# Optimization experiments

Measured on AMD Instinct MI355X. Metric: run time of the kernel, lower is better.

## Reference

```python
import jax, jax.numpy as jnp
import numpy as np

NUM_HEADS = 4
D_MODEL = 256
HEAD_DIM = D_MODEL // NUM_HEADS  # 64
B, N = 4, 2048


def _pointwise_conv(w, b, x):
    # Conv1d(kernel_size=1): x [b, in, n] -> [b, out, n]
    return jnp.einsum('oi,bin->bon', w, x) + b[None, :, None]


def setup_inputs() -> dict:
    key = jax.random.key(0)
    ks = jax.random.split(key, 11)
    def g(k, shape, scale=1.0):
        return jax.random.normal(k, shape, dtype=jnp.float32) * scale
    return {
        'query': g(ks[0], (B, D_MODEL, N)),
        'key':   g(ks[1], (B, D_MODEL, N)),
        'value': g(ks[2], (B, D_MODEL, N)),
        'wq': g(ks[3], (D_MODEL, D_MODEL), 1.0 / np.sqrt(D_MODEL)),
        'bq': g(ks[4], (D_MODEL,), 0.02),
        'wk': g(ks[5], (D_MODEL, D_MODEL), 1.0 / np.sqrt(D_MODEL)),
        'bk': g(ks[6], (D_MODEL,), 0.02),
        'wv': g(ks[7], (D_MODEL, D_MODEL), 1.0 / np.sqrt(D_MODEL)),
        'bv': g(ks[8], (D_MODEL,), 0.02),
        'wm': g(ks[9], (D_MODEL, D_MODEL), 1.0 / np.sqrt(D_MODEL)),
        'bm': g(ks[10], (D_MODEL,), 0.02),
    }


def reference(query, key, value, wq, bq, wk, bk, wv, bv, wm, bm):
    b = query.shape[0]
    # Project and split heads: [b, d_model, n] -> [b, head_dim, heads, n]
    q = _pointwise_conv(wq, bq, query).reshape(b, HEAD_DIM, NUM_HEADS, -1)
    k = _pointwise_conv(wk, bk, key).reshape(b, HEAD_DIM, NUM_HEADS, -1)
    v = _pointwise_conv(wv, bv, value).reshape(b, HEAD_DIM, NUM_HEADS, -1)
    # scaled dot-product attention; scale is head dim (query.shape[1] in torch)
    scores = jnp.einsum('bdhn,bdhm->bhnm', q, k) / jnp.sqrt(jnp.float32(HEAD_DIM))
    prob = jax.nn.softmax(scores, axis=-1)
    x = jnp.einsum('bhnm,bdhm->bdhn', prob, v)
    # merge heads and final pointwise conv
    x = x.reshape(b, HEAD_DIM * NUM_HEADS, -1)
    return _pointwise_conv(wm, bm, x)
```

## Files before the change

kernel.cpp:

```cpp
#include <hip/hip_runtime.h>

typedef __attribute__((ext_vector_type(8))) short short8;
typedef __attribute__((ext_vector_type(4))) float f32x4;
typedef __attribute__((ext_vector_type(16))) float f32x16;

#define MFMA_B16(a, b, c) __builtin_amdgcn_mfma_f32_16x16x32_bf16((a), (b), (c), 0, 0, 0)
#define MFMA32(a, b, c) __builtin_amdgcn_mfma_f32_32x32x16_bf16((a), (b), (c), 0, 0, 0)

#define NTOK 2048
#define DM 256
#define NB4 4
#define HD 64

__device__ __forceinline__ short f2bf(float f) {
  union { float f; unsigned u; } x;
  x.f = f;
  unsigned r = x.u + 0x7fffu + ((x.u >> 16) & 1u);
  return (short)(r >> 16);
}
__device__ __forceinline__ float bf2f(short s) {
  union { unsigned u; float f; } x;
  x.u = ((unsigned)(unsigned short)s) << 16;
  return x.f;
}

__device__ __forceinline__ void gload16(const short* g, short* l) {
  __builtin_amdgcn_global_load_lds(
      (const __attribute__((address_space(1))) void*)g,
      (__attribute__((address_space(3))) void*)l, 16, 0, 0);
}

__global__ __launch_bounds__(256) void k_wpre(const float* __restrict__ w0,
    const float* __restrict__ w1, const float* __restrict__ w2,
    const float* __restrict__ w3, short* __restrict__ wbf) {
  int t = blockIdx.x * 256 + threadIdx.x;
  const float* ws4[4] = {w0, w1, w2, w3};
  int base = t * 32;
#pragma unroll
  for (int blk = 0; blk < 4; blk++) {
    int off = base + blk * 8;
    int tau = off >> 16;
    int rest = off & 65535;
    int c = rest >> 8, ip = rest & 255;
    const float* srow = ws4[tau] + (size_t)c * 256;
    short8 r;
#pragma unroll
    for (int j = 0; j < 8; j++) {
      int i2 = ip + j;
      r[j] = (tau == 3) ? f2bf(srow[4 * (i2 & 63) + (i2 >> 6)]) : f2bf(srow[i2]);
    }
    *(short8*)(wbf + off) = r;
  }
}

__global__ __launch_bounds__(256, 4) void k_proj(const float* __restrict__ q,
    const float* __restrict__ k, const float* __restrict__ v,
    const short* __restrict__ wbf, const float* __restrict__ bq,
    const float* __restrict__ bk, const float* __restrict__ bv,
    short* __restrict__ qt, short* __restrict__ kt, short* __restrict__ vt) {
  __shared__ __align__(16) short As[16384];
  int z = blockIdx.y, b = z & 3, tau = z >> 2;
  const float* src = ((tau == 0) ? q : (tau == 1) ? k : v) + (size_t)b * DM * NTOK;
  const short* W = wbf + (size_t)tau * 65536;
  const float* bias = (tau == 0) ? bq : (tau == 1) ? bk : bv;
  int n0 = blockIdx.x * 64;
  int t = threadIdx.x;
  {
    int nseg = t & 15, rg = t >> 4;
#pragma unroll
    for (int outer = 0; outer < 2; outer++) {
      int iG = rg + 16 * outer;
      const float* s0 = src + (size_t)(iG * 8) * NTOK + n0 + nseg * 4;
      float4 rows[8];
#pragma unroll
      for (int j = 0; j < 8; j++) rows[j] = *(const float4*)(s0 + (size_t)j * NTOK);
      int i32 = iG >> 2, fhi = iG & 3, s = iG & 7;
#pragma unroll
      for (int e = 0; e < 4; e++) {
        int n = nseg * 4 + e;
        int nb = n >> 4, flo = n & 15;
        short8 r;
#pragma unroll
        for (int j = 0; j < 8; j++)
          r[j] = f2bf(e == 0 ? rows[j].x : e == 1 ? rows[j].y
                                         : e == 2 ? rows[j].z : rows[j].w);
        int frag = ((nb * 8 + i32) * 64 + fhi * 16 + flo) ^ s;
        *(short8*)(As + frag * 8) = r;
      }
    }
  }
  __syncthreads();
  int lane = t & 63, w = t >> 6;
  int lo = lane & 15, hi = lane >> 4;
  f32x4 acc[4][4] = {};
  const short* wrow = W + (size_t)(64 * w + lo) * DM + hi * 8;
#pragma unroll
  for (int ks = 0; ks < 8; ks++) {
    int sr = hi | ((ks & 1) << 2);
    short8 xf[4];
#pragma unroll
    for (int nb = 0; nb < 4; nb++) {
      int frag = ((nb * 8 + ks) * 64 + lane) ^ sr;
      xf[nb] = *(const short8*)(As + frag * 8);
    }
#pragma unroll
    for (int cb = 0; cb < 4; cb++) {
      short8 wf = *(const short8*)(wrow + (size_t)cb * 16 * DM + ks * 32);
      if (tau < 2) {
#pragma unroll
        for (int nb = 0; nb < 4; nb++)
          acc[cb][nb] = MFMA_B16(xf[nb], wf, acc[cb][nb]);
      } else {
#pragma unroll
        for (int nb = 0; nb < 4; nb++)
          acc[cb][nb] = MFMA_B16(wf, xf[nb], acc[cb][nb]);
      }
    }
  }
  if (tau < 2) {
    short* out = tau ? kt : qt;
    float scale = tau ? 1.0f : (0.125f * 1.44269504f);
#pragma unroll
    for (int cb = 0; cb < 4; cb++) {
      int c = 64 * w + 16 * cb + lo;
      float bvv = bias[c];
      int h = c & 3, d = c >> 2;
      size_t base = (size_t)(b * 4 + h) * 64;
#pragma unroll
      for (int nb = 0; nb < 4; nb++) {
#pragma unroll
        for (int r = 0; r < 4; r++) {
          int n = n0 + 16 * nb + 4 * hi + r;
          size_t addr = (((base + (n >> 5)) * 4 + (d >> 4)) * 64 +
                         (n & 31) + 32 * ((d >> 3) & 1)) * 8 + (d & 7);
          out[addr] = f2bf((acc[cb][nb][r] + bvv) * scale);
        }
      }
    }
  } else {
#pragma unroll
    for (int cb = 0; cb < 4; cb++) {
#pragma unroll
      for (int r = 0; r < 4; r++) {
        int c = 64 * w + 16 * cb + 4 * hi + r;
        float bvv = bias[c];
        int h = c & 3, d = c >> 2;
        size_t base = (size_t)(b * 4 + h) * 128;
#pragma unroll
        for (int nb = 0; nb < 4; nb++) {
          int m = n0 + 16 * nb + lo;
          size_t addr = (((base + (m >> 4)) * 2 + (d >> 5)) * 64 +
                         (d & 31) + 32 * ((m >> 3) & 1)) * 8 + (m & 7);
          vt[addr] = f2bf(acc[cb][nb][r] + bvv);
        }
      }
    }
  }
}

template <int SPLIT>
__global__ __launch_bounds__(512, 4) void k_attn(const short* __restrict__ qt,
    const short* __restrict__ kt, const short* __restrict__ vt,
    short* __restrict__ opart, float* __restrict__ ml) {
  __shared__ __align__(16) short Ks[3][4096];
  __shared__ __align__(16) short Vs[3][4096];
  int b, h, chunk, n0;
  if (SPLIT == 4) {
    int bid = blockIdx.x;
    int xcd = bid & 7, slot = bid >> 3;
    int g = xcd + 8 * (slot >> 3);
    n0 = (slot & 7) * 256;
    h = g & 3;
    int zz = g >> 2;
    b = zz & 3;
    chunk = zz >> 2;
  } else {
    b = blockIdx.z & 3; chunk = 0; h = blockIdx.y; n0 = blockIdx.x * 256;
  }
  int tid = threadIdx.x;
  int lane = tid & 63, w = tid >> 6;
  int l31 = lane & 31, hi2 = lane >> 5;
  const int CH = NTOK / SPLIT;
  const int kv0 = chunk * CH;
  int bh = b * 4 + h;
  const short* Qf = qt + (size_t)bh * 131072;
  const short* Kf = kt + (size_t)bh * 131072;
  const short* Vf = vt + (size_t)bh * 131072;
  short8 qf[4];
#pragma unroll
  for (int dk = 0; dk < 4; dk++)
    qf[dk] = *(const short8*)(Qf + (((size_t)((n0 >> 5) + w) * 4 + dk) * 64 + lane) * 8);
  f32x16 acc[2] = {};
  float lacc = 0.0f;

  const int nt = CH >> 6;
  {
    int m0 = kv0;
    gload16(Kf + (size_t)(m0 >> 5) * 2048 + tid * 8, &Ks[0][tid * 8]);
    gload16(Vf + (size_t)(m0 >> 4) * 1024 + tid * 8, &Vs[0][tid * 8]);
    int m1 = kv0 + 64;
    gload16(Kf + (size_t)(m1 >> 5) * 2048 + tid * 8, &Ks[1][tid * 8]);
    gload16(Vf + (size_t)(m1 >> 4) * 1024 + tid * 8, &Vs[1][tid * 8]);
  }
  asm volatile("s_waitcnt vmcnt(0)" ::: "memory");
  __builtin_amdgcn_s_barrier();
  __builtin_amdgcn_sched_barrier(0);

#pragma unroll
  for (int t = 0; t < nt; t++) {
    int cur = t % 3;
    if (t + 2 < nt) {
      int m2 = kv0 + ((t + 2) << 6);
      int nxt = (t + 2) % 3;
      gload16(Kf + (size_t)(m2 >> 5) * 2048 + tid * 8, &Ks[nxt][tid * 8]);
      gload16(Vf + (size_t)(m2 >> 4) * 1024 + tid * 8, &Vs[nxt][tid * 8]);
    }
#pragma unroll
    for (int mb2 = 0; mb2 < 2; mb2++) {
      f32x16 s = {};
      __builtin_amdgcn_s_setprio(1);
#pragma unroll
      for (int dk = 0; dk < 4; dk++) {
        short8 kf = *(const short8*)&Ks[cur][(mb2 * 4 + dk) * 512 + lane * 8];
        s = MFMA32(kf, qf[dk], s);
      }
      __builtin_amdgcn_s_setprio(0);
#pragma unroll
      for (int ks = 0; ks < 2; ks++) {
        float e0 = exp2f(s[ks * 8 + 0]), e1 = exp2f(s[ks * 8 + 1]);
        float e2 = exp2f(s[ks * 8 + 2]), e3 = exp2f(s[ks * 8 + 3]);
        float e4 = exp2f(s[ks * 8 + 4]), e5 = exp2f(s[ks * 8 + 5]);
        float e6 = exp2f(s[ks * 8 + 6]), e7 = exp2f(s[ks * 8 + 7]);
        lacc += ((e0 + e1) + (e2 + e3)) + ((e4 + e5) + (e6 + e7));
        unsigned A, B, C2, D2;
        asm("v_cvt_pk_bf16_f32 %0, %1, %2" : "=v"(A) : "v"(e0), "v"(e1));
        asm("v_cvt_pk_bf16_f32 %0, %1, %2" : "=v"(C2) : "v"(e2), "v"(e3));
        asm("v_cvt_pk_bf16_f32 %0, %1, %2" : "=v"(B) : "v"(e4), "v"(e5));
        asm("v_cvt_pk_bf16_f32 %0, %1, %2" : "=v"(D2) : "v"(e6), "v"(e7));
        asm("v_permlane32_swap_b32 %0, %1" : "+v"(A), "+v"(B));
        asm("v_permlane32_swap_b32 %0, %1" : "+v"(C2), "+v"(D2));
        union { unsigned u[4]; short8 v8; } pu;
        pu.u[0] = A; pu.u[1] = C2; pu.u[2] = B; pu.u[3] = D2;
        __builtin_amdgcn_s_setprio(1);
#pragma unroll
        for (int dcol = 0; dcol < 2; dcol++) {
          short8 vf = *(const short8*)&Vs[cur][((mb2 * 2 + ks) * 2 + dcol) * 512 + lane * 8];
          acc[dcol] = MFMA32(pu.v8, vf, acc[dcol]);
        }
        __builtin_amdgcn_s_setprio(0);
      }
    }
    if (t + 1 < nt) {
      if (t + 2 < nt)
        asm volatile("s_waitcnt vmcnt(2) lgkmcnt(0)" ::: "memory");
      else
        asm volatile("s_waitcnt vmcnt(0) lgkmcnt(0)" ::: "memory");
      __builtin_amdgcn_s_barrier();
      __builtin_amdgcn_sched_barrier(0);
    }
  }

  float l = lacc + __shfl_xor(lacc, 32);
  size_t rbase = (((size_t)chunk * NB4 + b) * 4 + h) * NTOK;
  if (lane < 32) ml[rbase + n0 + 32 * w + lane] = l;
#pragma unroll
  for (int r = 0; r < 16; r++) {
    int n = n0 + 32 * w + (r & 3) + 8 * (r >> 2) + 4 * hi2;
#pragma unroll
    for (int dcol = 0; dcol < 2; dcol++)
      opart[(rbase + n) * HD + dcol * 32 + l31] = f2bf(acc[dcol][r]);
  }
}

template <int NCH>
__global__ __launch_bounds__(256, 4) void k_out(const short* __restrict__ W,
    const short* __restrict__ opart, const float* __restrict__ ml,
    const float* __restrict__ bias, float* __restrict__ outp) {
  __shared__ __align__(16) short As[8192];
  int b = blockIdx.y;
  int n0 = blockIdx.x * 32;
  int t = threadIdx.x;
  int lane = t & 63, w = t >> 6;
  int lo16 = lane & 15, hi = lane >> 4;
  {
    int d8 = t & 7, h = (t >> 3) & 3, nb8 = t >> 5;
    int i32 = 2 * h + (d8 >> 2), fhi = d8 & 3;
#pragma unroll
    for (int it = 0; it < 4; it++) {
      int noff = nb8 * 4 + it;
      int n = n0 + noff;
      int nb = noff >> 4, flo = noff & 15;
      size_t row0 = ((size_t)b * 4 + h) * NTOK + n;
      float l = ml[row0];
      float o[8];
      short8 o0 = *(const short8*)(opart + row0 * HD + d8 * 8);
#pragma unroll
      for (int j = 0; j < 8; j++) o[j] = bf2f(o0[j]);
#pragma unroll
      for (int ch = 1; ch < NCH; ch++) {
        size_t rowc = row0 + (size_t)ch * 16 * NTOK;
        l += ml[rowc];
        short8 oc = *(const short8*)(opart + rowc * HD + d8 * 8);
#pragma unroll
        for (int j = 0; j < 8; j++) o[j] += bf2f(oc[j]);
      }
      float inv = 1.0f / l;
      short8 res;
#pragma unroll
      for (int j = 0; j < 8; j++) res[j] = f2bf(o[j] * inv);
      int frag = ((nb * 8 + i32) * 64 + fhi * 16 + flo) ^ d8;
      *(short8*)(As + frag * 8) = res;
    }
  }
  __syncthreads();
  f32x4 acc[4][2] = {};
  const short* arow = W + (size_t)(64 * w + lo16) * DM + hi * 8;
#pragma unroll
  for (int ks = 0; ks < 8; ks++) {
    int sr = hi | ((ks & 1) << 2);
    short8 bbr[2];
#pragma unroll
    for (int nb = 0; nb < 2; nb++) {
      int frag = ((nb * 8 + ks) * 64 + lane) ^ sr;
      bbr[nb] = *(const short8*)(As + frag * 8);
    }
#pragma unroll
    for (int cb = 0; cb < 4; cb++) {
      short8 a = *(const short8*)(arow + (size_t)cb * 16 * DM + ks * 32);
#pragma unroll
      for (int nb = 0; nb < 2; nb++)
        acc[cb][nb] = MFMA_B16(a, bbr[nb], acc[cb][nb]);
    }
  }
#pragma unroll
  for (int cb = 0; cb < 4; cb++) {
#pragma unroll
    for (int r = 0; r < 4; r++) {
      int c = 64 * w + 16 * cb + 4 * hi + r;
      float bvv = bias[c];
#pragma unroll
      for (int nb = 0; nb < 2; nb++) {
        int n = n0 + 16 * nb + lo16;
        outp[((size_t)b * DM + c) * NTOK + n] = acc[cb][nb][r] + bvv;
      }
    }
  }
}

extern "C" void kernel_launch(void* const* d_in, const int* in_sizes, int n_in,
                              void* d_out, int out_size, void* d_ws, size_t ws_size,
                              hipStream_t stream) {
  const float* q  = (const float*)d_in[0];
  const float* k  = (const float*)d_in[1];
  const float* v  = (const float*)d_in[2];
  const float* wq = (const float*)d_in[3];
  const float* bq = (const float*)d_in[4];
  const float* wk = (const float*)d_in[5];
  const float* bk = (const float*)d_in[6];
  const float* wv = (const float*)d_in[7];
  const float* bv = (const float*)d_in[8];
  const float* wm = (const float*)d_in[9];
  const float* bm = (const float*)d_in[10];

  char* ws = (char*)d_ws;
  const size_t MB = 1024 * 1024;
  short* Qt  = (short*)(ws);
  short* Kt  = (short*)(ws + 4 * MB);
  short* Vt  = (short*)(ws + 8 * MB);
  short* Wbf = (short*)(ws + 12 * MB);
  float* ML    = (float*)(ws + 13 * MB);
  short* Opart = (short*)(ws + 14 * MB);

  k_wpre<<<dim3(32), 256, 0, stream>>>(wq, wk, wv, wm, Wbf);
  k_proj<<<dim3(32, 12), 256, 0, stream>>>(q, k, v, Wbf, bq, bk, bv, Qt, Kt, Vt);

  if (ws_size >= 32 * MB) {
    k_attn<4><<<dim3(512), 512, 0, stream>>>(Qt, Kt, Vt, Opart, ML);
    k_out<4><<<dim3(64, 4), 256, 0, stream>>>(Wbf + 3 * 65536, Opart, ML, bm, (float*)d_out);
  } else {
    k_attn<1><<<dim3(8, 4, 4), 512, 0, stream>>>(Qt, Kt, Vt, Opart, ML);
    k_out<1><<<dim3(64, 4), 256, 0, stream>>>(Wbf + 3 * 65536, Opart, ML, bm, (float*)d_out);
  }

  (void)in_sizes; (void)n_in; (void)out_size; (void)ws_size;
}
```

Measured before the change: 68.22 us.

## Fuse split-KV combine and output projection into attention via last-block counter

Removes the separate k_out launch on the split path. Each attention block atomically increments a per-(batch, query-tile) counter, and the last of the 16 contributing blocks (4 heads x 4 KV chunks) merges the partial outputs, normalizes them, and applies the output pointwise conv with bias directly to the output. This saves a kernel launch and the gap between the two kernels. In exchange it adds a memset, threadfences and atomics, and a serial tail in which only 32 of 512 blocks do the projection work.

```diff
diff --git a/kernel.cpp b/kernel.cpp
--- a/kernel.cpp
+++ b/kernel.cpp
@@ -161,9 +161,13 @@
 template <int SPLIT>
 __global__ __launch_bounds__(512, 4) void k_attn(const short* __restrict__ qt,
     const short* __restrict__ kt, const short* __restrict__ vt,
-    short* __restrict__ opart, float* __restrict__ ml) {
-  __shared__ __align__(16) short Ks[3][4096];
-  __shared__ __align__(16) short Vs[3][4096];
+    short* __restrict__ opart, float* __restrict__ ml,
+    const short* __restrict__ Wm, const float* __restrict__ bm,
+    float* __restrict__ outp, int* __restrict__ cnt) {
+  __shared__ __align__(16) short SMEM[24576];
+  __shared__ int winflag;
+  short (*Ks)[4096] = (short(*)[4096])SMEM;
+  short (*Vs)[4096] = (short(*)[4096])(SMEM + 12288);
   int b, h, chunk, n0;
   if (SPLIT == 4) {
     int bid = blockIdx.x;
@@ -270,6 +274,89 @@
     for (int dcol = 0; dcol < 2; dcol++)
       opart[(rbase + n) * HD + dcol * 32 + l31] = f2bf(acc[dcol][r]);
   }
+
+  if (SPLIT != 4) return;
+
+  __threadfence();
+  __syncthreads();
+  int g = b * 8 + (n0 >> 8);
+  if (tid == 0) winflag = (atomicAdd(&cnt[g], 1) == 15);
+  __syncthreads();
+  if (!winflag) return;
+  __threadfence();
+
+  int half = tid >> 8, t2 = tid & 255;
+  short* Ao = SMEM + half * 8192;
+  int lane2 = t2 & 63, w2 = t2 >> 6;
+  int lo16 = lane2 & 15, hi = lane2 >> 4;
+#pragma unroll 1
+  for (int qi = 0; qi < 4; qi++) {
+    int n0u = n0 + qi * 64 + 32 * half;
+    {
+      int d8 = t2 & 7, hh = (t2 >> 3) & 3, nb8 = t2 >> 5;
+      int i32 = 2 * hh + (d8 >> 2), fhi = d8 & 3;
+#pragma unroll
+      for (int it = 0; it < 4; it++) {
+        int noff = nb8 * 4 + it;
+        int n = n0u + noff;
+        int nb = noff >> 4, flo = noff & 15;
+        size_t row0 = ((size_t)b * 4 + hh) * NTOK + n;
+        float lr = ml[row0];
+        float o[8];
+        short8 o0 = *(const short8*)(opart + row0 * HD + d8 * 8);
+#pragma unroll
+        for (int j = 0; j < 8; j++) o[j] = bf2f(o0[j]);
+#pragma unroll
+        for (int ch = 1; ch < 4; ch++) {
+          size_t rowc = row0 + (size_t)ch * 16 * NTOK;
+          lr += ml[rowc];
+          short8 oc = *(const short8*)(opart + rowc * HD + d8 * 8);
+#pragma unroll
+          for (int j = 0; j < 8; j++) o[j] += bf2f(oc[j]);
+        }
+        float inv = 1.0f / lr;
+        short8 res;
+#pragma unroll
+        for (int j = 0; j < 8; j++) res[j] = f2bf(o[j] * inv);
+        int frag = ((nb * 8 + i32) * 64 + fhi * 16 + flo) ^ d8;
+        *(short8*)(Ao + frag * 8) = res;
+      }
+    }
+    __syncthreads();
+    f32x4 acc2[4][2] = {};
+    const short* arow = Wm + (size_t)(64 * w2 + lo16) * DM + hi * 8;
+#pragma unroll
+    for (int ks = 0; ks < 8; ks++) {
+      int sr = hi | ((ks & 1) << 2);
+      short8 bbr[2];
+#pragma unroll
+      for (int nb = 0; nb < 2; nb++) {
+        int frag = ((nb * 8 + ks) * 64 + lane2) ^ sr;
+        bbr[nb] = *(const short8*)(Ao + frag * 8);
+      }
+#pragma unroll
+      for (int cb = 0; cb < 4; cb++) {
+        short8 a = *(const short8*)(arow + (size_t)cb * 16 * DM + ks * 32);
+#pragma unroll
+        for (int nb = 0; nb < 2; nb++)
+          acc2[cb][nb] = MFMA_B16(a, bbr[nb], acc2[cb][nb]);
+      }
+    }
+#pragma unroll
+    for (int cb = 0; cb < 4; cb++) {
+#pragma unroll
+      for (int r = 0; r < 4; r++) {
+        int c = 64 * w2 + 16 * cb + 4 * hi + r;
+        float bvv = bm[c];
+#pragma unroll
+        for (int nb = 0; nb < 2; nb++) {
+          int n = n0u + 16 * nb + lo16;
+          outp[((size_t)b * DM + c) * NTOK + n] = acc2[cb][nb][r] + bvv;
+        }
+      }
+    }
+    __syncthreads();
+  }
 }
 
 template <int NCH>
@@ -369,16 +456,19 @@
   short* Vt  = (short*)(ws + 8 * MB);
   short* Wbf = (short*)(ws + 12 * MB);
   float* ML    = (float*)(ws + 13 * MB);
+  int*   CNT   = (int*)(ws + 13 * MB + 768 * 1024);
   short* Opart = (short*)(ws + 14 * MB);
 
+  hipMemsetAsync(CNT, 0, 32 * sizeof(int), stream);
   k_wpre<<<dim3(32), 256, 0, stream>>>(wq, wk, wv, wm, Wbf);
   k_proj<<<dim3(32, 12), 256, 0, stream>>>(q, k, v, Wbf, bq, bk, bv, Qt, Kt, Vt);
 
   if (ws_size >= 32 * MB) {
-    k_attn<4><<<dim3(512), 512, 0, stream>>>(Qt, Kt, Vt, Opart, ML);
-    k_out<4><<<dim3(64, 4), 256, 0, stream>>>(Wbf + 3 * 65536, Opart, ML, bm, (float*)d_out);
+    k_attn<4><<<dim3(512), 512, 0, stream>>>(Qt, Kt, Vt, Opart, ML,
+        Wbf + 3 * 65536, bm, (float*)d_out, CNT);
   } else {
-    k_attn<1><<<dim3(8, 4, 4), 512, 0, stream>>>(Qt, Kt, Vt, Opart, ML);
+    k_attn<1><<<dim3(8, 4, 4), 512, 0, stream>>>(Qt, Kt, Vt, Opart, ML,
+        Wbf + 3 * 65536, bm, (float*)d_out, CNT);
     k_out<1><<<dim3(64, 4), 256, 0, stream>>>(Wbf + 3 * 65536, Opart, ML, bm, (float*)d_out);
   }
 
```

Result: slower. 250.4 us (+267.0%).
